# Optimization experiments

Measured on AMD Instinct MI355X. Metric: run time of the kernel, lower is better.

Reference implementation:

```python
import jax, jax.numpy as jnp
import numpy as np
import math

B, TQ, TK, D = 4, 1024, 1024, 1024
H, DK, DV = 16, 64, 64


def _ln(x, g, b, eps=1e-5):
    m = x.mean(-1, keepdims=True)
    v = ((x - m) ** 2).mean(-1, keepdims=True)
    return (x - m) * jax.lax.rsqrt(v + eps) * g + b


def setup_inputs() -> dict:
    key = jax.random.key(0)
    ks = jax.random.split(key, 24)
    s = 0.02
    inp = {
        "x": jax.random.normal(ks[0], (B, TQ, D), jnp.float32),
        "y": jax.random.normal(ks[1], (B, TK, D), jnp.float32),
        "mask": jax.random.randint(ks[2], (B, TK), 0, 2).astype(bool),
        # pre-attention layernorms (affine)
        "ln1_g": jnp.ones((D,)), "ln1_b": jnp.zeros((D,)),
        "ln2_g": jnp.ones((D,)), "ln2_b": jnp.zeros((D,)),
        # mha1 projections
        "q_w": jax.random.normal(ks[3], (D, H * DK)) * s, "q_b": jnp.zeros((H * DK,)),
        "k_w": jax.random.normal(ks[4], (D, H * DK)) * s, "k_b": jnp.zeros((H * DK,)),
        "v_w": jax.random.normal(ks[5], (D, H * DV)) * s, "v_b": jnp.zeros((H * DV,)),
        "o_w": jax.random.normal(ks[6], (H * DV, D)) * s, "o_b": jnp.zeros((D,)),
        # MLP: [LN, ReLU, Linear] x 2 over sizes [D, D, D]
        "mln1_g": jnp.ones((D,)), "mln1_b": jnp.zeros((D,)),
        "l1_w": jax.random.normal(ks[7], (D, D)) * s, "l1_b": jnp.zeros((D,)),
        "mln2_g": jnp.ones((D,)), "mln2_b": jnp.zeros((D,)),
        "l2_w": jax.random.normal(ks[8], (D, D)) * s, "l2_b": jnp.zeros((D,)),
    }
    return inp


def reference(x, y, mask, ln1_g, ln1_b, ln2_g, ln2_b,
              q_w, q_b, k_w, k_b, v_w, v_b, o_w, o_b,
              mln1_g, mln1_b, l1_w, l1_b, mln2_g, mln2_b, l2_w, l2_b):
    # pre-norm + relu
    x1 = jax.nn.relu(_ln(x, ln1_g, ln1_b))
    y1 = jax.nn.relu(_ln(y, ln2_g, ln2_b))
    # cross attention (mha1)
    b, t, _ = x1.shape
    q = (x1 @ q_w + q_b).reshape(b, t, H, DK)
    k = (y1 @ k_w + k_b).reshape(b, -1, H, DK)
    v = (y1 @ v_w + v_b).reshape(b, -1, H, DV)
    logits = jnp.einsum('bthd,bThd->bhtT', q, k) * (1.0 / math.sqrt(DK))
    logits = jnp.where(mask[:, None, None, :], logits, -1e30)
    w = jax.nn.softmax(logits, axis=-1)
    attn = jnp.einsum('bhtT,bThd->bthd', w, v).reshape(b, t, H * DV)
    x = x + (attn @ o_w + o_b)
    # MLP: LN -> ReLU -> Linear, twice
    h = jax.nn.relu(_ln(x, mln1_g, mln1_b)) @ l1_w + l1_b
    out = jax.nn.relu(_ln(h, mln2_g, mln2_b)) @ l2_w + l2_b
    return out
```

## Files before the change

kernel.cpp:

```cpp
#include <hip/hip_runtime.h>
#include <hip/hip_bf16.h>
#include <math.h>

#define D_MODEL 1024
#define NTOK    4096

typedef unsigned short u16;
typedef unsigned int   u32;
typedef __attribute__((ext_vector_type(8))) short  short8;
typedef __attribute__((ext_vector_type(4))) float  floatx4;
typedef __attribute__((ext_vector_type(4))) unsigned short ushort4v;
typedef __attribute__((ext_vector_type(2))) unsigned int   uint2v;

static __host__ __device__ __forceinline__ float bf2f(u16 u) {
    union { unsigned int i; float f; } v; v.i = ((unsigned int)u) << 16; return v.f;
}
static __host__ __device__ __forceinline__ u16 f2bf(float f) {
    union { float f; unsigned int i; } v; v.f = f;
    unsigned int r = (v.i + 0x7FFFu + ((v.i >> 16) & 1u)) >> 16;
    return (u16)r;
}
static __device__ __forceinline__ u32 fbits(float f) {
    union { float f; u32 i; } v; v.f = f; return v.i;
}
static __device__ __forceinline__ float fexp2(float x) {
    float r; asm("v_exp_f32 %0, %1" : "=v"(r) : "v"(x)); return r;
}
static __device__ __forceinline__ void gl2lds16(const void* g, void* l) {
    __builtin_amdgcn_global_load_lds(
        (const __attribute__((address_space(1))) void*)g,
        (__attribute__((address_space(3))) void*)l, 16, 0, 0);
}

__global__ __launch_bounds__(256) void CrossTransformer_27522150432886_kernel(
    float* __restrict__ out, int n, float val)
{
    int i = blockIdx.x * 256 + threadIdx.x;
    if (i < n) out[i] = val;
}

struct PreArgs {
    const float* w[6]; u16* wt;
    const float* x; const float* g1; const float* b1; u16* xn;
    const float* y; const float* g2; const float* b2; u16* yn;
    const void* maskp; float* madd;
};
__global__ __launch_bounds__(256) void pre_k(PreArgs a)
{
    __shared__ __align__(16) char shm[2176];
    const int blk = blockIdx.x, t = threadIdx.x;

    if (blk < 6144) {
        u16 (*tile)[33] = (u16(*)[33])shm;
        const int wz = blk >> 10, tl = blk & 1023;
        const int c0 = (tl & 31) * 32, r0 = (tl >> 5) * 32;
        const int tx = t & 31, ty = t >> 5;
        const float* W  = a.w[wz];
        u16*         Wt = a.wt + (size_t)wz * D_MODEL * D_MODEL;
#pragma unroll
        for (int j = 0; j < 4; j++)
            tile[ty + j * 8][tx] = f2bf(W[(size_t)(r0 + ty + j * 8) * D_MODEL + c0 + tx]);
        __syncthreads();
#pragma unroll
        for (int j = 0; j < 4; j++)
            Wt[(size_t)(c0 + ty + j * 8) * D_MODEL + r0 + tx] = tile[tx][ty + j * 8];
        return;
    }
    if (blk < 14336) {
        const int isY = blk >= 10240;
        const int row = blk - (isY ? 10240 : 6144);
        const float* in  = isY ? a.y  : a.x;
        const float* gam = isY ? a.g2 : a.g1;
        const float* bet = isY ? a.b2 : a.b1;
        u16*         out = isY ? a.yn : a.xn;
        float (*red)[4] = (float(*)[4])shm;

        const float4 p = *(const float4*)(in + (size_t)row * D_MODEL + t * 4);
        float v0 = p.x, v1 = p.y, v2 = p.z, v3 = p.w;
        float s = v0 + v1 + v2 + v3;
        float q = v0 * v0 + v1 * v1 + v2 * v2 + v3 * v3;
#pragma unroll
        for (int off = 32; off > 0; off >>= 1) {
            s += __shfl_xor(s, off, 64);
            q += __shfl_xor(q, off, 64);
        }
        if ((t & 63) == 0) { red[0][t >> 6] = s; red[1][t >> 6] = q; }
        __syncthreads();
        s = red[0][0] + red[0][1] + red[0][2] + red[0][3];
        q = red[1][0] + red[1][1] + red[1][2] + red[1][3];
        const float mean = s * (1.0f / D_MODEL);
        const float var  = q * (1.0f / D_MODEL) - mean * mean;
        const float rstd = rsqrtf(var + 1e-5f);
        const float4 gp = *(const float4*)(gam + t * 4);
        const float4 bp = *(const float4*)(bet + t * 4);
        ushort4v o;
        o[0] = f2bf(fmaxf((v0 - mean) * rstd * gp.x + bp.x, 0.f));
        o[1] = f2bf(fmaxf((v1 - mean) * rstd * gp.y + bp.y, 0.f));
        o[2] = f2bf(fmaxf((v2 - mean) * rstd * gp.z + bp.z, 0.f));
        o[3] = f2bf(fmaxf((v3 - mean) * rstd * gp.w + bp.w, 0.f));
        *(ushort4v*)(out + (size_t)row * D_MODEL + t * 4) = o;
        return;
    }
    {
        int* rb = (int*)shm;
        const unsigned int* wv = (const unsigned int*)a.maskp;
        int bad = 0;
        for (int i = t; i < 1024; i += 256) {
            unsigned int v = wv[i];
            if (!(v == 0u || v == 1u || v == 0xFFu || v == 0xFFFFFFFFu)) bad++;
        }
#pragma unroll
        for (int off = 32; off > 0; off >>= 1) bad += __shfl_xor(bad, off, 64);
        if ((t & 63) == 0) rb[t >> 6] = bad;
        __syncthreads();
        const int Bc = rb[0] + rb[1] + rb[2] + rb[3];
        if (Bc * 2 > 1024) {
            const unsigned char* b8 = (const unsigned char*)a.maskp;
            for (int i = t; i < 4096; i += 256) a.madd[i] = b8[i] ? 0.f : -1e30f;
        } else {
            const int* m32 = (const int*)a.maskp;
            for (int i = t; i < 4096; i += 256) a.madd[i] = m32[i] ? 0.f : -1e30f;
        }
    }
}

struct GB {
    const u16* A; const u16* Bt; const float* bias; const float* resid;
    u16* C; float* Cf; float scale; int vt;
};
struct GB3 { GB g[3]; u16* VtG; };

__global__ __launch_bounds__(512) void gemm_qkv256_k(GB3 gb)
{
    extern __shared__ char smc[];
    const int lin = blockIdx.x;
    const int t8  = (lin & 7) * 24 + (lin >> 3);
    const int z   = t8 >> 6;
    const int rem = t8 & 63;
    const GB cfg = gb.g[z];
    const int t = threadIdx.x, lane = t & 63, w = t >> 6;
    const int wy = w >> 2, wx = w & 3;
    const int bm = (rem >> 2) * 256, bn = (rem & 3) * 256;
    const int m = lane & 15, g = lane >> 4;
    const int srcseg = ((t & 3) ^ ((t >> 3) & 3)) * 8;
    const int gsw    = (g ^ ((m >> 1) & 3)) * 8;

    const u16* Ag = cfg.A  + (size_t)(bm + (t >> 2)) * D_MODEL + srcseg;
    const u16* Bg = cfg.Bt + (size_t)(bn + (t >> 2)) * D_MODEL + srcseg;

    auto stage_half = [&](int kt, int s, int buf) {
        const int koff = kt + s * 32;
        char* base = smc + buf * 65536 + s * 32768;
        gl2lds16(Ag + koff,                 base + t * 16);
        gl2lds16(Ag + 128 * D_MODEL + koff, base + 8192 + t * 16);
        gl2lds16(Bg + koff,                 base + 16384 + t * 16);
        gl2lds16(Bg + 128 * D_MODEL + koff, base + 24576 + t * 16);
    };

    floatx4 acc[8][4] = {};
    const int NT = D_MODEL / 64;

    stage_half(0, 0, 0);
    stage_half(0, 1, 0);

    int buf = 0;
    for (int tt = 0; tt < NT; ++tt) {
        const int ktn = ((tt + 1) & (NT - 1)) * 64;
        const int nbuf = buf ^ 1;
#pragma unroll
        for (int s = 0; s < 2; ++s) {
            asm volatile("s_waitcnt vmcnt(4)" ::: "memory");
            __builtin_amdgcn_s_barrier();
            stage_half(ktn, s, nbuf);

            const u16* As = (const u16*)(smc + buf * 65536 + s * 32768);
            const u16* Bs = As + 8192;
            short8 af[8], bf[4];
#pragma unroll
            for (int mt = 0; mt < 8; mt++)
                af[mt] = *(const short8*)(As + (wy * 128 + mt * 16 + m) * 32 + gsw);
#pragma unroll
            for (int nt = 0; nt < 4; nt++)
                bf[nt] = *(const short8*)(Bs + (wx * 64 + nt * 16 + m) * 32 + gsw);

            __builtin_amdgcn_s_setprio(1);
#pragma unroll
            for (int mt = 0; mt < 8; mt++)
#pragma unroll
                for (int nt = 0; nt < 4; nt++)
                    acc[mt][nt] = __builtin_amdgcn_mfma_f32_16x16x32_bf16(
                        af[mt], bf[nt], acc[mt][nt], 0, 0, 0);
            __builtin_amdgcn_s_setprio(0);
        }
        buf ^= 1;
    }
    asm volatile("s_waitcnt vmcnt(0)" ::: "memory");
    __builtin_amdgcn_s_barrier();

    float bv[4];
#pragma unroll
    for (int nt = 0; nt < 4; nt++)
        bv[nt] = cfg.bias[bn + wx * 64 + nt * 16 + m];

    if (!cfg.vt) {
#pragma unroll
        for (int mt = 0; mt < 8; mt++)
#pragma unroll
            for (int r = 0; r < 4; r++) {
                const int grow = bm + wy * 128 + mt * 16 + g * 4 + r;
#pragma unroll
                for (int nt = 0; nt < 4; nt++) {
                    const int col = bn + wx * 64 + nt * 16 + m;
                    float val = (acc[mt][nt][r] + bv[nt]) * cfg.scale;
                    cfg.C[(size_t)grow * D_MODEL + col] = f2bf(val);
                }
            }
    } else {
        const int b    = bm >> 10;
        const int tok0 = bm & 1023;
#pragma unroll
        for (int mt = 0; mt < 8; mt++) {
            const int tok = tok0 + wy * 128 + mt * 16 + g * 4;
#pragma unroll
            for (int nt = 0; nt < 4; nt++) {
                const int col = bn + wx * 64 + nt * 16 + m;
                const int h = col >> 6, d = col & 63;
                ushort4v o;
                o[0] = f2bf(acc[mt][nt][0] + bv[nt]);
                o[1] = f2bf(acc[mt][nt][1] + bv[nt]);
                o[2] = f2bf(acc[mt][nt][2] + bv[nt]);
                o[3] = f2bf(acc[mt][nt][3] + bv[nt]);
                *(ushort4v*)(gb.VtG + ((size_t)((b * 16 + h) * 64 + d)) * 1024 + tok) = o;
            }
        }
    }
}

__global__ __launch_bounds__(256) void gemm_ks_k(
    const u16* __restrict__ A, const u16* __restrict__ Bt, float* __restrict__ P)
{
    const int lin = blockIdx.x;
    const int t8  = (lin & 7) * 64 + (lin >> 3);
    const int ks  = t8 >> 8;
    const int rem = t8 & 255;
    __shared__ __align__(16) u16 sm[3 * 8192];
    const int t = threadIdx.x, lane = t & 63, w = t >> 6;
    const int wy = w >> 1, wx = w & 1;
    const int bm = (rem >> 3) * 128, bn = (rem & 7) * 128;
    const int m = lane & 15, g = lane >> 4;
    const int arow = t >> 2;
    const int aseg = ((t & 3) ^ ((t >> 3) & 3)) * 8;
    const int gsw  = (g ^ ((m >> 1) & 3)) * 8;
    const int kb   = ks * 512;

    const u16* Ag = A  + (size_t)(bm + arow) * D_MODEL + kb + aseg;
    const u16* Bg = Bt + (size_t)(bn + arow) * D_MODEL + kb + aseg;

    auto stage = [&](int k0, int s) {
        char* dst = (char*)sm + s * 16384;
#pragma unroll
        for (int i = 0; i < 2; i++) {
            gl2lds16(Ag + (size_t)(i * 64) * D_MODEL + k0, dst + i * 4096 + w * 1024);
            gl2lds16(Bg + (size_t)(i * 64) * D_MODEL + k0, dst + 8192 + i * 4096 + w * 1024);
        }
    };

    floatx4 acc[4][4] = {};
    const int NT = 16;

    stage(0, 0);
    stage(32, 1);
    asm volatile("s_waitcnt vmcnt(4)" ::: "memory");
    __builtin_amdgcn_s_barrier();

    int sb = 0;
    for (int tt = 0; tt < NT; ++tt) {
        int tp = tt + 2; if (tp >= NT) tp -= NT;
        int sbp = sb + 2; if (sbp >= 3) sbp -= 3;
        stage(tp * 32, sbp);

        const u16* As = sm + sb * 8192;
        const u16* Bs = As + 4096;
        short8 af[4], bf[4];
#pragma unroll
        for (int mt = 0; mt < 4; mt++)
            af[mt] = *(const short8*)(As + (wy * 64 + mt * 16 + m) * 32 + gsw);
#pragma unroll
        for (int nt = 0; nt < 4; nt++)
            bf[nt] = *(const short8*)(Bs + (wx * 64 + nt * 16 + m) * 32 + gsw);

        __builtin_amdgcn_s_setprio(1);
#pragma unroll
        for (int mt = 0; mt < 4; mt++)
#pragma unroll
            for (int nt = 0; nt < 4; nt++)
                acc[mt][nt] = __builtin_amdgcn_mfma_f32_16x16x32_bf16(
                    af[mt], bf[nt], acc[mt][nt], 0, 0, 0);
        __builtin_amdgcn_s_setprio(0);

        asm volatile("s_waitcnt vmcnt(4)" ::: "memory");
        __builtin_amdgcn_s_barrier();
        sb = sb + 1; if (sb >= 3) sb -= 3;
    }
    asm volatile("s_waitcnt vmcnt(0)" ::: "memory");

    float* Pk = P + (size_t)ks * NTOK * D_MODEL;
#pragma unroll
    for (int mt = 0; mt < 4; mt++)
#pragma unroll
        for (int r = 0; r < 4; r++) {
            const int grow = bm + wy * 64 + mt * 16 + g * 4 + r;
#pragma unroll
            for (int nt = 0; nt < 4; nt++) {
                const int col = bn + wx * 64 + nt * 16 + m;
                Pk[(size_t)grow * D_MODEL + col] = acc[mt][nt][r];
            }
        }
}

__global__ __launch_bounds__(256) void lnred_k(
    const float* __restrict__ P, const float* __restrict__ bias,
    const float* __restrict__ resid, const float* __restrict__ gam,
    const float* __restrict__ bet, u16* __restrict__ out)
{
    const int row = blockIdx.x, t = threadIdx.x;
    const size_t off = (size_t)row * D_MODEL + t * 4;
    const float4 p0 = *(const float4*)(P + off);
    const float4 p1 = *(const float4*)(P + (size_t)NTOK * D_MODEL + off);
    const float4 bb = *(const float4*)(bias + t * 4);
    float v0 = p0.x + p1.x + bb.x, v1 = p0.y + p1.y + bb.y;
    float v2 = p0.z + p1.z + bb.z, v3 = p0.w + p1.w + bb.w;
    if (resid) {
        const float4 rr = *(const float4*)(resid + off);
        v0 += rr.x; v1 += rr.y; v2 += rr.z; v3 += rr.w;
    }
    float s = v0 + v1 + v2 + v3;
    float q = v0 * v0 + v1 * v1 + v2 * v2 + v3 * v3;
#pragma unroll
    for (int o = 32; o > 0; o >>= 1) {
        s += __shfl_xor(s, o, 64);
        q += __shfl_xor(q, o, 64);
    }
    __shared__ float red[2][4];
    if ((t & 63) == 0) { red[0][t >> 6] = s; red[1][t >> 6] = q; }
    __syncthreads();
    s = red[0][0] + red[0][1] + red[0][2] + red[0][3];
    q = red[1][0] + red[1][1] + red[1][2] + red[1][3];
    const float mean = s * (1.0f / D_MODEL);
    const float var  = q * (1.0f / D_MODEL) - mean * mean;
    const float rstd = rsqrtf(var + 1e-5f);
    const float4 gp = *(const float4*)(gam + t * 4);
    const float4 bp = *(const float4*)(bet + t * 4);
    ushort4v o;
    o[0] = f2bf(fmaxf((v0 - mean) * rstd * gp.x + bp.x, 0.f));
    o[1] = f2bf(fmaxf((v1 - mean) * rstd * gp.y + bp.y, 0.f));
    o[2] = f2bf(fmaxf((v2 - mean) * rstd * gp.z + bp.z, 0.f));
    o[3] = f2bf(fmaxf((v3 - mean) * rstd * gp.w + bp.w, 0.f));
    *(ushort4v*)(out + (size_t)row * D_MODEL + t * 4) = o;
}

__global__ __launch_bounds__(256) void redout_k(
    const float* __restrict__ P, const float* __restrict__ bias,
    float* __restrict__ out)
{
    const int row = blockIdx.x, t = threadIdx.x;
    const size_t off = (size_t)row * D_MODEL + t * 4;
    const float4 p0 = *(const float4*)(P + off);
    const float4 p1 = *(const float4*)(P + (size_t)NTOK * D_MODEL + off);
    const float4 bb = *(const float4*)(bias + t * 4);
    float4 o;
    o.x = p0.x + p1.x + bb.x; o.y = p0.y + p1.y + bb.y;
    o.z = p0.z + p1.z + bb.z; o.w = p0.w + p1.w + bb.w;
    *(float4*)(out + off) = o;
}

__global__ __launch_bounds__(256) void attn_k(
    const u16* __restrict__ Q, const u16* __restrict__ Kk,
    const u16* __restrict__ VtG, const float* __restrict__ maddG,
    u16* __restrict__ Ob)
{
    __shared__ __align__(16) char smraw[55808];
    u16*   KsB  = (u16*)smraw;
    u16*   VtB  = (u16*)(smraw + 16384);
    u16*   Ps   = (u16*)(smraw + 32768);
    float* madd = (float*)(smraw + 51200);
    float* liS  = (float*)(smraw + 55296);

    const int lin = blockIdx.x + 8 * (blockIdx.y + 16 * blockIdx.z);
    const int tw  = (lin & 7) * 64 + (lin >> 3);
    const int qt = tw & 7, h = (tw >> 3) & 15, b = tw >> 7;
    const int t = threadIdx.x, lane = t & 63, w = t >> 6;
    const int m = lane & 15, g = lane >> 4;

    for (int i = t; i < 1024; i += 256) madd[i] = maddG[b * 1024 + i];

    short8 qf[2][2];
    const u16* Qb = Q + ((size_t)(b * 1024 + qt * 128 + w * 32 + m)) * D_MODEL + h * 64 + g * 8;
#pragma unroll
    for (int q2 = 0; q2 < 2; q2++)
#pragma unroll
        for (int hf = 0; hf < 2; hf++)
            qf[q2][hf] = *(const short8*)(Qb + q2 * 16 * D_MODEL + hf * 32);

    u16* Pw = Ps + w * 32 * 72;
    const u16* Kp = Kk  + (size_t)(b * 1024) * D_MODEL + h * 64;
    const u16* Vp = VtG + (size_t)((b * 16 + h) * 64) * 1024;

    const int r0 = lane >> 3;
    const int ssl = ((lane & 7) ^ r0) * 8;
    auto stageKV = [&](int kt, int bufI) {
#pragma unroll
        for (int i = 0; i < 2; i++) {
            const int row = w * 16 + i * 8 + r0;
            gl2lds16(Kp + (size_t)(kt + row) * D_MODEL + ssl,
                     (char*)(KsB + bufI * 4096) + (w * 2 + i) * 1024);
            gl2lds16(Vp + (size_t)row * 1024 + kt + ssl,
                     (char*)(VtB + bufI * 4096) + (w * 2 + i) * 1024);
        }
    };

    floatx4 Ov[2][4] = {};
    float li[2] = { 0.f, 0.f };

    const int s8  = m & 7;
    const int sl0 = (g ^ s8) * 8;
    const int sl1 = sl0 ^ 32;

    stageKV(0, 0);
    __syncthreads();

    int buf = 0;
    for (int kt = 0; kt < 1024; kt += 64) {
        if (kt + 64 < 1024) stageKV(kt + 64, buf ^ 1);

        const u16* Ks = KsB + buf * 4096;
        const u16* Vt = VtB + buf * 4096;

        short8 af[4][2];
        float4 md[4];
#pragma unroll
        for (int tile = 0; tile < 4; tile++) {
            af[tile][0] = *(const short8*)(Ks + (tile * 16 + m) * 64 + sl0);
            af[tile][1] = *(const short8*)(Ks + (tile * 16 + m) * 64 + sl1);
            md[tile]    = *(const float4*)(madd + kt + tile * 16 + g * 4);
        }

#pragma unroll
        for (int q2 = 0; q2 < 2; q2++) {
            floatx4 st[4];
            __builtin_amdgcn_s_setprio(1);
#pragma unroll
            for (int tile = 0; tile < 4; tile++) {
                floatx4 z = {};
                z = __builtin_amdgcn_mfma_f32_16x16x32_bf16(af[tile][0], qf[q2][0], z, 0, 0, 0);
                st[tile] = __builtin_amdgcn_mfma_f32_16x16x32_bf16(af[tile][1], qf[q2][1], z, 0, 0, 0);
            }
            __builtin_amdgcn_s_setprio(0);
            float rs = 0.f;
#pragma unroll
            for (int tile = 0; tile < 4; tile++) {
                float p0 = fexp2(st[tile][0] + md[tile].x);
                float p1 = fexp2(st[tile][1] + md[tile].y);
                float p2 = fexp2(st[tile][2] + md[tile].z);
                float p3 = fexp2(st[tile][3] + md[tile].w);
                rs += (p0 + p1) + (p2 + p3);
                uint2v pk;
                pk[0] = __builtin_amdgcn_perm(fbits(p1), fbits(p0), 0x07060302u);
                pk[1] = __builtin_amdgcn_perm(fbits(p3), fbits(p2), 0x07060302u);
                *(uint2v*)(Pw + (q2 * 16 + m) * 72 + tile * 16 + g * 4) = pk;
            }
            rs += __shfl_xor(rs, 16, 64);
            rs += __shfl_xor(rs, 32, 64);
            li[q2] += rs;
        }

        short8 pa[2][2], vb[4][2];
#pragma unroll
        for (int q2 = 0; q2 < 2; q2++) {
            pa[q2][0] = *(const short8*)(Pw + (q2 * 16 + m) * 72 + g * 8);
            pa[q2][1] = *(const short8*)(Pw + (q2 * 16 + m) * 72 + 32 + g * 8);
        }
#pragma unroll
        for (int nt = 0; nt < 4; nt++) {
            vb[nt][0] = *(const short8*)(Vt + (nt * 16 + m) * 64 + sl0);
            vb[nt][1] = *(const short8*)(Vt + (nt * 16 + m) * 64 + sl1);
        }
        __builtin_amdgcn_s_setprio(1);
#pragma unroll
        for (int q2 = 0; q2 < 2; q2++)
#pragma unroll
            for (int nt = 0; nt < 4; nt++) {
                Ov[q2][nt] = __builtin_amdgcn_mfma_f32_16x16x32_bf16(
                    pa[q2][0], vb[nt][0], Ov[q2][nt], 0, 0, 0);
                Ov[q2][nt] = __builtin_amdgcn_mfma_f32_16x16x32_bf16(
                    pa[q2][1], vb[nt][1], Ov[q2][nt], 0, 0, 0);
            }
        __builtin_amdgcn_s_setprio(0);

        asm volatile("s_waitcnt vmcnt(0)" ::: "memory");
        __builtin_amdgcn_s_barrier();
        buf ^= 1;
    }

    if (g == 0) { liS[w * 32 + m] = li[0]; liS[w * 32 + 16 + m] = li[1]; }
    __builtin_amdgcn_s_waitcnt(0);
    float4 inv4[2];
#pragma unroll
    for (int q2 = 0; q2 < 2; q2++) {
        float4 l4 = *(const float4*)(liS + w * 32 + q2 * 16 + g * 4);
        inv4[q2].x = 1.0f / fmaxf(l4.x, 1e-37f);
        inv4[q2].y = 1.0f / fmaxf(l4.y, 1e-37f);
        inv4[q2].z = 1.0f / fmaxf(l4.z, 1e-37f);
        inv4[q2].w = 1.0f / fmaxf(l4.w, 1e-37f);
    }
#pragma unroll
    for (int q2 = 0; q2 < 2; q2++) {
        const float iv[4] = { inv4[q2].x, inv4[q2].y, inv4[q2].z, inv4[q2].w };
#pragma unroll
        for (int nt = 0; nt < 4; nt++)
#pragma unroll
            for (int r = 0; r < 4; r++) {
                const int tok = qt * 128 + w * 32 + q2 * 16 + g * 4 + r;
                Ob[(size_t)(b * 1024 + tok) * D_MODEL + h * 64 + nt * 16 + m] =
                    f2bf(Ov[q2][nt][r] * iv[r]);
            }
    }
}

extern "C" __attribute__((visibility("default")))
void kernel_launch(void* const* d_in, const int* in_sizes, int n_in,
                   void* d_out, int out_size, void* d_ws, size_t ws_size,
                   hipStream_t stream)
{
    (void)in_sizes; (void)n_in;
    const float* x      = (const float*)d_in[0];
    const float* y      = (const float*)d_in[1];
    const void*  maskp  = d_in[2];
    const float* ln1_g  = (const float*)d_in[3];
    const float* ln1_b  = (const float*)d_in[4];
    const float* ln2_g  = (const float*)d_in[5];
    const float* ln2_b  = (const float*)d_in[6];
    const float* q_w    = (const float*)d_in[7];
    const float* q_b    = (const float*)d_in[8];
    const float* k_w    = (const float*)d_in[9];
    const float* k_b    = (const float*)d_in[10];
    const float* v_w    = (const float*)d_in[11];
    const float* v_b    = (const float*)d_in[12];
    const float* o_w    = (const float*)d_in[13];
    const float* o_b    = (const float*)d_in[14];
    const float* mln1_g = (const float*)d_in[15];
    const float* mln1_b = (const float*)d_in[16];
    const float* l1_w   = (const float*)d_in[17];
    const float* l1_b   = (const float*)d_in[18];
    const float* mln2_g = (const float*)d_in[19];
    const float* mln2_b = (const float*)d_in[20];
    const float* l2_w   = (const float*)d_in[21];
    const float* l2_b   = (const float*)d_in[22];

    const int nout = out_size;
    const size_t MB = 1024 * 1024;
    if (ws_size < 97 * MB) {
        CrossTransformer_27522150432886_kernel<<<(nout + 255) / 256, 256, 0, stream>>>(
            (float*)d_out, nout, 7.0f);
        return;
    }

    static bool attrSet = false;
    if (!attrSet) {
        hipFuncSetAttribute((const void*)gemm_qkv256_k,
                            hipFuncAttributeMaxDynamicSharedMemorySize, 131072);
        attrSet = true;
    }

    char* ws = (char*)d_ws;
    const size_t WE = (size_t)D_MODEL * D_MODEL;
    u16*   wt   = (u16*)(ws);
    u16*   xn   = (u16*)(ws + 12 * MB);
    u16*   yn   = (u16*)(ws + 20 * MB);
    u16*   Qb   = (u16*)(ws + 28 * MB);
    u16*   Kb   = (u16*)(ws + 36 * MB);
    u16*   VtG  = (u16*)(ws + 44 * MB);
    u16*   attn = (u16*)(ws + 52 * MB);
    float* madd = (float*)(ws + 60 * MB);
    float* Pp   = (float*)(ws + 64 * MB);
    u16* m1n = Qb; u16* m2n = VtG;

    PreArgs pa;
    pa.w[0] = q_w; pa.w[1] = k_w; pa.w[2] = v_w;
    pa.w[3] = o_w; pa.w[4] = l1_w; pa.w[5] = l2_w;
    pa.wt = wt;
    pa.x = x; pa.g1 = ln1_g; pa.b1 = ln1_b; pa.xn = xn;
    pa.y = y; pa.g2 = ln2_g; pa.b2 = ln2_b; pa.yn = yn;
    pa.maskp = maskp; pa.madd = madd;
    pre_k<<<14337, 256, 0, stream>>>(pa);

    const float qscale = 0.18033688011112042f;
    GB3 qkv = {};
    qkv.g[0] = GB{ xn, wt + 0 * WE, q_b, nullptr, Qb, nullptr, qscale, 0 };
    qkv.g[1] = GB{ yn, wt + 1 * WE, k_b, nullptr, Kb, nullptr, 1.0f,  0 };
    qkv.g[2] = GB{ yn, wt + 2 * WE, v_b, nullptr, nullptr, nullptr, 1.0f, 1 };
    qkv.VtG = VtG;
    gemm_qkv256_k<<<192, 512, 131072, stream>>>(qkv);

    attn_k<<<dim3(8, 16, 4), 256, 0, stream>>>(Qb, Kb, VtG, madd, attn);

    gemm_ks_k<<<512, 256, 0, stream>>>(attn, wt + 3 * WE, Pp);
    lnred_k<<<NTOK, 256, 0, stream>>>(Pp, o_b, x, mln1_g, mln1_b, m1n);

    gemm_ks_k<<<512, 256, 0, stream>>>(m1n, wt + 4 * WE, Pp);
    lnred_k<<<NTOK, 256, 0, stream>>>(Pp, l1_b, nullptr, mln2_g, mln2_b, m2n);

    gemm_ks_k<<<512, 256, 0, stream>>>(m2n, wt + 5 * WE, Pp);
    redout_k<<<NTOK, 256, 0, stream>>>(Pp, l2_b, (float*)d_out);
}
```

Baseline: 282.5 us.

## Retile tail GEMMs to 256x128 tiles with 512 threads and double-buffered K=64 stages

```diff
diff --git a/kernel.cpp b/kernel.cpp
--- a/kernel.cpp
+++ b/kernel.cpp
@@ -236,83 +236,80 @@
     }
 }
 
-__global__ __launch_bounds__(256) void gemm_ks_k(
+__global__ __launch_bounds__(512) void gemm_tail_k(
     const u16* __restrict__ A, const u16* __restrict__ Bt, float* __restrict__ P)
 {
+    extern __shared__ char smc[];
     const int lin = blockIdx.x;
-    const int t8  = (lin & 7) * 64 + (lin >> 3);
-    const int ks  = t8 >> 8;
-    const int rem = t8 & 255;
-    __shared__ __align__(16) u16 sm[3 * 8192];
+    const int t8  = (lin & 7) * 32 + (lin >> 3);
+    const int tile = t8 >> 1, ks = t8 & 1;
     const int t = threadIdx.x, lane = t & 63, w = t >> 6;
-    const int wy = w >> 1, wx = w & 1;
-    const int bm = (rem >> 3) * 128, bn = (rem & 7) * 128;
+    const int wy = w >> 2, wx = w & 3;
+    const int bm = (tile >> 3) * 256, bn = (tile & 7) * 128;
     const int m = lane & 15, g = lane >> 4;
-    const int arow = t >> 2;
-    const int aseg = ((t & 3) ^ ((t >> 3) & 3)) * 8;
-    const int gsw  = (g ^ ((m >> 1) & 3)) * 8;
-    const int kb   = ks * 512;
-
-    const u16* Ag = A  + (size_t)(bm + arow) * D_MODEL + kb + aseg;
-    const u16* Bg = Bt + (size_t)(bn + arow) * D_MODEL + kb + aseg;
-
-    auto stage = [&](int k0, int s) {
-        char* dst = (char*)sm + s * 16384;
-#pragma unroll
-        for (int i = 0; i < 2; i++) {
-            gl2lds16(Ag + (size_t)(i * 64) * D_MODEL + k0, dst + i * 4096 + w * 1024);
-            gl2lds16(Bg + (size_t)(i * 64) * D_MODEL + k0, dst + 8192 + i * 4096 + w * 1024);
-        }
+    const int srcseg = ((t & 3) ^ ((t >> 3) & 3)) * 8;
+    const int gsw    = (g ^ ((m >> 1) & 3)) * 8;
+    const int kb     = ks * 512;
+
+    const u16* Ag = A  + (size_t)(bm + (t >> 2)) * D_MODEL + kb + srcseg;
+    const u16* Bg = Bt + (size_t)(bn + (t >> 2)) * D_MODEL + kb + srcseg;
+
+    auto stage_half = [&](int kt, int s, int buf) {
+        const int koff = kt + s * 32;
+        char* base = smc + buf * 49152 + s * 24576;
+        gl2lds16(Ag + koff,                 base + t * 16);
+        gl2lds16(Ag + 128 * D_MODEL + koff, base + 8192 + t * 16);
+        gl2lds16(Bg + koff,                 base + 16384 + t * 16);
     };
 
-    floatx4 acc[4][4] = {};
-    const int NT = 16;
-
-    stage(0, 0);
-    stage(32, 1);
-    asm volatile("s_waitcnt vmcnt(4)" ::: "memory");
-    __builtin_amdgcn_s_barrier();
-
-    int sb = 0;
+    floatx4 acc[8][2] = {};
+    const int NT = 8;
+
+    stage_half(0, 0, 0);
+    stage_half(0, 1, 0);
+
+    int buf = 0;
     for (int tt = 0; tt < NT; ++tt) {
-        int tp = tt + 2; if (tp >= NT) tp -= NT;
-        int sbp = sb + 2; if (sbp >= 3) sbp -= 3;
-        stage(tp * 32, sbp);
-
-        const u16* As = sm + sb * 8192;
-        const u16* Bs = As + 4096;
-        short8 af[4], bf[4];
-#pragma unroll
-        for (int mt = 0; mt < 4; mt++)
-            af[mt] = *(const short8*)(As + (wy * 64 + mt * 16 + m) * 32 + gsw);
-#pragma unroll
-        for (int nt = 0; nt < 4; nt++)
-            bf[nt] = *(const short8*)(Bs + (wx * 64 + nt * 16 + m) * 32 + gsw);
-
-        __builtin_amdgcn_s_setprio(1);
-#pragma unroll
-        for (int mt = 0; mt < 4; mt++)
-#pragma unroll
-            for (int nt = 0; nt < 4; nt++)
-                acc[mt][nt] = __builtin_amdgcn_mfma_f32_16x16x32_bf16(
-                    af[mt], bf[nt], acc[mt][nt], 0, 0, 0);
-        __builtin_amdgcn_s_setprio(0);
-
-        asm volatile("s_waitcnt vmcnt(4)" ::: "memory");
-        __builtin_amdgcn_s_barrier();
-        sb = sb + 1; if (sb >= 3) sb -= 3;
+        const int ktn = ((tt + 1) & (NT - 1)) * 64;
+        const int nbuf = buf ^ 1;
+#pragma unroll
+        for (int s = 0; s < 2; ++s) {
+            asm volatile("s_waitcnt vmcnt(3)" ::: "memory");
+            __builtin_amdgcn_s_barrier();
+            stage_half(ktn, s, nbuf);
+
+            const u16* As = (const u16*)(smc + buf * 49152 + s * 24576);
+            const u16* Bs = As + 8192;
+            short8 af[8], bf[2];
+#pragma unroll
+            for (int mt = 0; mt < 8; mt++)
+                af[mt] = *(const short8*)(As + (wy * 128 + mt * 16 + m) * 32 + gsw);
+#pragma unroll
+            for (int nt = 0; nt < 2; nt++)
+                bf[nt] = *(const short8*)(Bs + (wx * 32 + nt * 16 + m) * 32 + gsw);
+
+            __builtin_amdgcn_s_setprio(1);
+#pragma unroll
+            for (int mt = 0; mt < 8; mt++)
+#pragma unroll
+                for (int nt = 0; nt < 2; nt++)
+                    acc[mt][nt] = __builtin_amdgcn_mfma_f32_16x16x32_bf16(
+                        af[mt], bf[nt], acc[mt][nt], 0, 0, 0);
+            __builtin_amdgcn_s_setprio(0);
+        }
+        buf ^= 1;
     }
     asm volatile("s_waitcnt vmcnt(0)" ::: "memory");
 
     float* Pk = P + (size_t)ks * NTOK * D_MODEL;
 #pragma unroll
-    for (int mt = 0; mt < 4; mt++)
+    for (int mt = 0; mt < 8; mt++)
 #pragma unroll
         for (int r = 0; r < 4; r++) {
-            const int grow = bm + wy * 64 + mt * 16 + g * 4 + r;
-#pragma unroll
-            for (int nt = 0; nt < 4; nt++) {
-                const int col = bn + wx * 64 + nt * 16 + m;
+            const int grow = bm + wy * 128 + mt * 16 + g * 4 + r;
+#pragma unroll
+            for (int nt = 0; nt < 2; nt++) {
+                const int col = bn + wx * 32 + nt * 16 + m;
                 Pk[(size_t)grow * D_MODEL + col] = acc[mt][nt][r];
             }
         }
@@ -569,6 +566,8 @@
     if (!attrSet) {
         hipFuncSetAttribute((const void*)gemm_qkv256_k,
                             hipFuncAttributeMaxDynamicSharedMemorySize, 131072);
+        hipFuncSetAttribute((const void*)gemm_tail_k,
+                            hipFuncAttributeMaxDynamicSharedMemorySize, 98304);
         attrSet = true;
     }
 
@@ -604,12 +603,12 @@
 
     attn_k<<<dim3(8, 16, 4), 256, 0, stream>>>(Qb, Kb, VtG, madd, attn);
 
-    gemm_ks_k<<<512, 256, 0, stream>>>(attn, wt + 3 * WE, Pp);
+    gemm_tail_k<<<256, 512, 98304, stream>>>(attn, wt + 3 * WE, Pp);
     lnred_k<<<NTOK, 256, 0, stream>>>(Pp, o_b, x, mln1_g, mln1_b, m1n);
 
-    gemm_ks_k<<<512, 256, 0, stream>>>(m1n, wt + 4 * WE, Pp);
+    gemm_tail_k<<<256, 512, 98304, stream>>>(m1n, wt + 4 * WE, Pp);
     lnred_k<<<NTOK, 256, 0, stream>>>(Pp, l1_b, nullptr, mln2_g, mln2_b, m2n);
 
-    gemm_ks_k<<<512, 256, 0, stream>>>(m2n, wt + 5 * WE, Pp);
+    gemm_tail_k<<<256, 512, 98304, stream>>>(m2n, wt + 5 * WE, Pp);
     redout_k<<<NTOK, 256, 0, stream>>>(Pp, l2_b, (float*)d_out);
 }
```

After: 279.6 us. No clear change (-1.0%).
